# Optimization experiments

Measured on AMD Instinct MI355X. Metric: run time of the kernel, lower is better.

## Reference

```python
import jax, jax.numpy as jnp
import numpy as np

N, M, D = 8192, 2048, 32


def setup_inputs() -> dict:
    key = jax.random.key(0)
    k1, k2, k3 = jax.random.split(key, 3)
    samples = jax.random.normal(k1, (N, D), dtype=jnp.float32)
    means = jax.random.normal(k2, (M, D), dtype=jnp.float32)
    # stds are divisors; keep them strictly positive, in [0.5, 1.5)
    stds = jax.random.uniform(k3, (M, D), dtype=jnp.float32) + 0.5
    return {"samples": samples, "means": means, "stds": stds}


def reference(samples, means, stds):
    # [N, M, D] broadcast pairwise weighted squared distance (full-buffer KDE)
    diff = means[None, :, :] - samples[:, None, :]
    logp = -0.5 * jnp.sum(jnp.square(diff) / stds[None, :, :], axis=2)  # [N, M]
    dist = jnp.mean(jnp.exp(logp), axis=1)  # [N]
    # invert=True branch: flip the density around its midrange
    dist = -dist + jnp.max(dist) + jnp.min(dist)
    return dist
```

## Files before the change

### kernel.cpp

```cpp
#include <hip/hip_runtime.h>

#define NS 8192
#define MS 2048
#define DD 32
#define MSPLIT 16
#define MCH 128
#define NITS 8
#define RBLK 32

typedef __attribute__((ext_vector_type(8))) short bf16x8;
typedef __attribute__((ext_vector_type(4))) float f32x4;
typedef unsigned short u16;
typedef unsigned int u32;

#define PART_OFF 0
#define MM_OFF   (MSPLIT * NS * 4)
#define CNT_OFF  (MM_OFF + 8)

__device__ inline float fast_exp2(float x) {
#if __has_builtin(__builtin_amdgcn_exp2f)
    return __builtin_amdgcn_exp2f(x);
#else
    return exp2f(x);
#endif
}
__device__ inline float fast_rcp(float x) {
#if __has_builtin(__builtin_amdgcn_rcpf)
    return __builtin_amdgcn_rcpf(x);
#else
    return 1.0f / x;
#endif
}

__device__ inline u32 cvt_pk_bf16(float a, float b) {
    u32 r;
    asm("v_cvt_pk_bf16_f32 %0, %1, %2" : "=v"(r) : "v"(a), "v"(b));
    return r;
}

__device__ inline void split8(const float* v, bf16x8& hi, bf16x8& lo) {
    union { u32 u[4]; bf16x8 b; } H, L;
#pragma unroll
    for (int j = 0; j < 4; ++j) {
        u32 h = cvt_pk_bf16(v[2 * j], v[2 * j + 1]);
        float ha = __uint_as_float(h << 16);
        float hb = __uint_as_float(h & 0xFFFF0000u);
        L.u[j] = cvt_pk_bf16(v[2 * j] - ha, v[2 * j + 1] - hb);
        H.u[j] = h;
    }
    hi = H.b;
    lo = L.b;
}

__global__ __launch_bounds__(256, 4) void kde_fused(const float* __restrict__ samples,
                                                    const float* __restrict__ means,
                                                    const float* __restrict__ stds,
                                                    unsigned char* __restrict__ wsb) {
    __shared__ u16 WBH[NITS * 512], WBL[NITS * 512], WCH[NITS * 512], WCL[NITS * 512];
    __shared__ float A2s[MCH];

    const int t = threadIdx.x;
    const int m0 = blockIdx.y * MCH;
    const float L2E = 1.4426950408889634f;

    if (blockIdx.x == 0 && blockIdx.y == 0 && t == 0) {
        unsigned* mm = (unsigned*)(wsb + MM_OFF);
        mm[0] = 0x7f7fffffu;
        mm[1] = 0u;
        *(unsigned*)(wsb + CNT_OFF) = 0u;
    }

    {
        const int ml = t >> 1, half = t & 1, d0 = half * 16;
        const float* mp = means + (size_t)(m0 + ml) * DD + d0;
        const float* vp = stds  + (size_t)(m0 + ml) * DD + d0;
        float mu[16], sd[16];
#pragma unroll
        for (int j = 0; j < 4; ++j) {
            float4 a4 = *(const float4*)(mp + j * 4);
            float4 c4 = *(const float4*)(vp + j * 4);
            mu[j*4+0]=a4.x; mu[j*4+1]=a4.y; mu[j*4+2]=a4.z; mu[j*4+3]=a4.w;
            sd[j*4+0]=c4.x; sd[j*4+1]=c4.y; sd[j*4+2]=c4.z; sd[j*4+3]=c4.w;
        }
        float Bv[16], Cv[16], a = 0.f;
#pragma unroll
        for (int j = 0; j < 16; ++j) {
            float inv = fast_rcp(sd[j]);
            Bv[j] = L2E * mu[j] * inv;
            Cv[j] = -0.5f * L2E * inv;
            a += mu[j] * mu[j] * inv;
        }
        a += __shfl_xor(a, 1);
        if (half == 0) A2s[ml] = -0.5f * L2E * a - 11.0f;

        const int it = ml >> 4, r15 = ml & 15;
#pragma unroll
        for (int r2 = 0; r2 < 2; ++r2) {
            bf16x8 bh, bl, ch, cl;
            split8(Bv + r2 * 8, bh, bl);
            split8(Cv + r2 * 8, ch, cl);
            const int qd = half * 2 + r2;
            const int base = ((it * 4 + qd) * 16 + r15) * 8;
            *(bf16x8*)&WBH[base] = bh;
            *(bf16x8*)&WBL[base] = bl;
            *(bf16x8*)&WCH[base] = ch;
            *(bf16x8*)&WCL[base] = cl;
        }
    }

    const int lane = t & 63, wid = t >> 6;
    const int r15 = lane & 15, g = lane >> 4;
    const int n0 = blockIdx.x * 256 + wid * 64;

    bf16x8 xh[4], xl[4], qh[4], ql[4];
#pragma unroll
    for (int nt = 0; nt < 4; ++nt) {
        const float* sp = samples + (size_t)(n0 + nt * 16 + r15) * DD + g * 8;
        float4 a4 = *(const float4*)sp, b4 = *(const float4*)(sp + 4);
        float xv[8] = {a4.x, a4.y, a4.z, a4.w, b4.x, b4.y, b4.z, b4.w};
        float qv[8];
#pragma unroll
        for (int j = 0; j < 8; ++j) qv[j] = xv[j] * xv[j];
        split8(xv, xh[nt], xl[nt]);
        split8(qv, qh[nt], ql[nt]);
    }

    __syncthreads();

    float rs[4] = {0.f, 0.f, 0.f, 0.f};

#pragma unroll 2
    for (int it = 0; it < NITS; ++it) {
        const int base = ((it * 4 + g) * 16 + r15) * 8;
        bf16x8 bh = *(const bf16x8*)&WBH[base];
        bf16x8 ch = *(const bf16x8*)&WCH[base];
        bf16x8 bl = *(const bf16x8*)&WBL[base];
        bf16x8 cl = *(const bf16x8*)&WCL[base];
        const f32x4 a2v = *(const f32x4*)&A2s[it * 16 + g * 4];
#pragma unroll
        for (int nt = 0; nt < 4; ++nt) {
            f32x4 acc = a2v;
            acc = __builtin_amdgcn_mfma_f32_16x16x32_bf16(bh, xh[nt], acc, 0, 0, 0);
            acc = __builtin_amdgcn_mfma_f32_16x16x32_bf16(ch, qh[nt], acc, 0, 0, 0);
            acc = __builtin_amdgcn_mfma_f32_16x16x32_bf16(bh, xl[nt], acc, 0, 0, 0);
            acc = __builtin_amdgcn_mfma_f32_16x16x32_bf16(ch, ql[nt], acc, 0, 0, 0);
            acc = __builtin_amdgcn_mfma_f32_16x16x32_bf16(bl, xh[nt], acc, 0, 0, 0);
            acc = __builtin_amdgcn_mfma_f32_16x16x32_bf16(cl, qh[nt], acc, 0, 0, 0);
            rs[nt] += (fast_exp2(acc[0]) + fast_exp2(acc[1]))
                    + (fast_exp2(acc[2]) + fast_exp2(acc[3]));
        }
    }

#pragma unroll
    for (int nt = 0; nt < 4; ++nt) {
        rs[nt] += __shfl_xor(rs[nt], 16);
        rs[nt] += __shfl_xor(rs[nt], 32);
    }

    float* partial = (float*)(wsb + PART_OFF);
    if (g == 0) {
#pragma unroll
        for (int nt = 0; nt < 4; ++nt)
            partial[(size_t)blockIdx.y * NS + n0 + nt * 16 + r15] = rs[nt];
    }
}

__global__ __launch_bounds__(256) void reduce_flip(unsigned char* __restrict__ wsb,
                                                   float* __restrict__ out) {
    const float* partial = (const float*)(wsb + PART_OFF);
    unsigned* mm = (unsigned*)(wsb + MM_OFF);
    unsigned* cnt = (unsigned*)(wsb + CNT_OFF);

    const int tid = threadIdx.x;
    const int n = blockIdx.x * 256 + tid;
    float v = 0.f;
#pragma unroll
    for (int j = 0; j < MSPLIT; ++j) v += partial[(size_t)j * NS + n];

    float mn = v, mx = v;
#pragma unroll
    for (int o = 1; o < 64; o <<= 1) {
        mn = fminf(mn, __shfl_xor(mn, o));
        mx = fmaxf(mx, __shfl_xor(mx, o));
    }
    __shared__ float smn[4], smx[4];
    __shared__ float sres[2];
    const int wv = tid >> 6, ln = tid & 63;
    if (ln == 0) { smn[wv] = mn; smx[wv] = mx; }
    __syncthreads();
    if (tid == 0) {
#pragma unroll
        for (int j = 1; j < 4; ++j) {
            mn = fminf(mn, smn[j]);
            mx = fmaxf(mx, smx[j]);
        }
        atomicMin(mm + 0, __float_as_uint(mn));
        atomicMax(mm + 1, __float_as_uint(mx));
        __threadfence();
        atomicAdd(cnt, 1u);
        while (__hip_atomic_load(cnt, __ATOMIC_ACQUIRE, __HIP_MEMORY_SCOPE_AGENT)
               < RBLK) {}
        sres[0] = __uint_as_float(
            __hip_atomic_load(mm + 0, __ATOMIC_RELAXED, __HIP_MEMORY_SCOPE_AGENT));
        sres[1] = __uint_as_float(
            __hip_atomic_load(mm + 1, __ATOMIC_RELAXED, __HIP_MEMORY_SCOPE_AGENT));
    }
    __syncthreads();
    out[n] = sres[1] + sres[0] - v;
}

extern "C" void kernel_launch(void* const* d_in, const int* in_sizes, int n_in,
                              void* d_out, int out_size, void* d_ws, size_t ws_size,
                              hipStream_t stream) {
    const float* samples = (const float*)d_in[0];
    const float* means   = (const float*)d_in[1];
    const float* stds    = (const float*)d_in[2];
    unsigned char* ws = (unsigned char*)d_ws;
    float* out = (float*)d_out;

    kde_fused<<<dim3(NS / 256, MSPLIT), 256, 0, stream>>>(samples, means, stds, ws);
    reduce_flip<<<dim3(RBLK), 256, 0, stream>>>(ws, out);
}
```

Before: 17.14 us.

## Switch KDE distance MFMA from 16x16x32 to 32x32x16 bf16 tiles

Replaces the 16x16x32 bf16 MFMA tiling with 32x32x16 MFMAs. Each wave now covers 32 samples by 32 means per tile, with the K=32 feature dimension split into two halves. The LDS weight layout, sample register fragments, A2 bias broadcast and the final cross-lane reduction are all restructured to match the new operand layout. The intent is fewer MFMA issues, less operand traffic and fewer shuffles. In exchange it uses more accumulator registers, so launch bounds are lowered from 4 to 2 blocks per SM.

```diff
diff --git a/kernel.cpp b/kernel.cpp
--- a/kernel.cpp
+++ b/kernel.cpp
@@ -5,11 +5,12 @@
 #define DD 32
 #define MSPLIT 16
 #define MCH 128
-#define NITS 8
+#define NIT32 4
 #define RBLK 32
 
 typedef __attribute__((ext_vector_type(8))) short bf16x8;
 typedef __attribute__((ext_vector_type(4))) float f32x4;
+typedef __attribute__((ext_vector_type(16))) float f32x16;
 typedef unsigned short u16;
 typedef unsigned int u32;
 
@@ -52,11 +53,11 @@
     lo = L.b;
 }
 
-__global__ __launch_bounds__(256, 4) void kde_fused(const float* __restrict__ samples,
+__global__ __launch_bounds__(256, 2) void kde_fused(const float* __restrict__ samples,
                                                     const float* __restrict__ means,
                                                     const float* __restrict__ stds,
                                                     unsigned char* __restrict__ wsb) {
-    __shared__ u16 WBH[NITS * 512], WBL[NITS * 512], WCH[NITS * 512], WCL[NITS * 512];
+    __shared__ u16 WBH[4096], WBL[4096], WCH[4096], WCL[4096];
     __shared__ float A2s[MCH];
 
     const int t = threadIdx.x;
@@ -71,9 +72,9 @@
     }
 
     {
-        const int ml = t >> 1, half = t & 1, d0 = half * 16;
-        const float* mp = means + (size_t)(m0 + ml) * DD + d0;
-        const float* vp = stds  + (size_t)(m0 + ml) * DD + d0;
+        const int ml = t >> 1, c = t & 1;
+        const float* mp = means + (size_t)(m0 + ml) * DD + c * 16;
+        const float* vp = stds  + (size_t)(m0 + ml) * DD + c * 16;
         float mu[16], sd[16];
 #pragma unroll
         for (int j = 0; j < 4; ++j) {
@@ -91,16 +92,15 @@
             a += mu[j] * mu[j] * inv;
         }
         a += __shfl_xor(a, 1);
-        if (half == 0) A2s[ml] = -0.5f * L2E * a - 11.0f;
-
-        const int it = ml >> 4, r15 = ml & 15;
-#pragma unroll
-        for (int r2 = 0; r2 < 2; ++r2) {
+        if (c == 0) A2s[ml] = -0.5f * L2E * a - 11.0f;
+
+        const int it = ml >> 5, r31 = ml & 31;
+#pragma unroll
+        for (int h5 = 0; h5 < 2; ++h5) {
             bf16x8 bh, bl, ch, cl;
-            split8(Bv + r2 * 8, bh, bl);
-            split8(Cv + r2 * 8, ch, cl);
-            const int qd = half * 2 + r2;
-            const int base = ((it * 4 + qd) * 16 + r15) * 8;
+            split8(Bv + h5 * 8, bh, bl);
+            split8(Cv + h5 * 8, ch, cl);
+            const int base = (((it * 2 + c) * 2 + h5) * 32 + r31) * 8;
             *(bf16x8*)&WBH[base] = bh;
             *(bf16x8*)&WBL[base] = bl;
             *(bf16x8*)&WCH[base] = ch;
@@ -109,59 +109,85 @@
     }
 
     const int lane = t & 63, wid = t >> 6;
-    const int r15 = lane & 15, g = lane >> 4;
-    const int n0 = blockIdx.x * 256 + wid * 64;
-
-    bf16x8 xh[4], xl[4], qh[4], ql[4];
-#pragma unroll
-    for (int nt = 0; nt < 4; ++nt) {
-        const float* sp = samples + (size_t)(n0 + nt * 16 + r15) * DD + g * 8;
-        float4 a4 = *(const float4*)sp, b4 = *(const float4*)(sp + 4);
-        float xv[8] = {a4.x, a4.y, a4.z, a4.w, b4.x, b4.y, b4.z, b4.w};
-        float qv[8];
-#pragma unroll
-        for (int j = 0; j < 8; ++j) qv[j] = xv[j] * xv[j];
-        split8(xv, xh[nt], xl[nt]);
-        split8(qv, qh[nt], ql[nt]);
+    const int r31 = lane & 31, h5 = lane >> 5;
+    const int n0w = blockIdx.x * 256 + wid * 64;
+
+    bf16x8 xh[2][2], xl[2][2], qh[2][2], ql[2][2];
+#pragma unroll
+    for (int nt = 0; nt < 2; ++nt) {
+        const float* sp = samples + (size_t)(n0w + nt * 32 + r31) * DD;
+#pragma unroll
+        for (int c = 0; c < 2; ++c) {
+            const float* p = sp + c * 16 + h5 * 8;
+            float4 a4 = *(const float4*)p, b4 = *(const float4*)(p + 4);
+            float xv[8] = {a4.x, a4.y, a4.z, a4.w, b4.x, b4.y, b4.z, b4.w};
+            float qv[8];
+#pragma unroll
+            for (int j = 0; j < 8; ++j) qv[j] = xv[j] * xv[j];
+            split8(xv, xh[nt][c], xl[nt][c]);
+            split8(qv, qh[nt][c], ql[nt][c]);
+        }
     }
 
     __syncthreads();
 
-    float rs[4] = {0.f, 0.f, 0.f, 0.f};
+    float rs[2] = {0.f, 0.f};
 
 #pragma unroll 2
-    for (int it = 0; it < NITS; ++it) {
-        const int base = ((it * 4 + g) * 16 + r15) * 8;
-        bf16x8 bh = *(const bf16x8*)&WBH[base];
-        bf16x8 ch = *(const bf16x8*)&WCH[base];
-        bf16x8 bl = *(const bf16x8*)&WBL[base];
-        bf16x8 cl = *(const bf16x8*)&WCL[base];
-        const f32x4 a2v = *(const f32x4*)&A2s[it * 16 + g * 4];
-#pragma unroll
-        for (int nt = 0; nt < 4; ++nt) {
-            f32x4 acc = a2v;
-            acc = __builtin_amdgcn_mfma_f32_16x16x32_bf16(bh, xh[nt], acc, 0, 0, 0);
-            acc = __builtin_amdgcn_mfma_f32_16x16x32_bf16(ch, qh[nt], acc, 0, 0, 0);
-            acc = __builtin_amdgcn_mfma_f32_16x16x32_bf16(bh, xl[nt], acc, 0, 0, 0);
-            acc = __builtin_amdgcn_mfma_f32_16x16x32_bf16(ch, ql[nt], acc, 0, 0, 0);
-            acc = __builtin_amdgcn_mfma_f32_16x16x32_bf16(bl, xh[nt], acc, 0, 0, 0);
-            acc = __builtin_amdgcn_mfma_f32_16x16x32_bf16(cl, qh[nt], acc, 0, 0, 0);
-            rs[nt] += (fast_exp2(acc[0]) + fast_exp2(acc[1]))
-                    + (fast_exp2(acc[2]) + fast_exp2(acc[3]));
-        }
-    }
-
-#pragma unroll
-    for (int nt = 0; nt < 4; ++nt) {
-        rs[nt] += __shfl_xor(rs[nt], 16);
-        rs[nt] += __shfl_xor(rs[nt], 32);
-    }
+    for (int it = 0; it < NIT32; ++it) {
+        bf16x8 wbh[2], wch[2], wbl[2], wcl[2];
+#pragma unroll
+        for (int c = 0; c < 2; ++c) {
+            const int base = (((it * 2 + c) * 2 + h5) * 32 + r31) * 8;
+            wbh[c] = *(const bf16x8*)&WBH[base];
+            wch[c] = *(const bf16x8*)&WCH[base];
+            wbl[c] = *(const bf16x8*)&WBL[base];
+            wcl[c] = *(const bf16x8*)&WCL[base];
+        }
+        f32x4 a2v[4];
+#pragma unroll
+        for (int p = 0; p < 4; ++p)
+            a2v[p] = *(const f32x4*)&A2s[it * 32 + p * 8 + h5 * 4];
+
+#pragma unroll
+        for (int nt = 0; nt < 2; ++nt) {
+            f32x16 acc;
+#pragma unroll
+            for (int p = 0; p < 4; ++p)
+#pragma unroll
+                for (int q = 0; q < 4; ++q) acc[p * 4 + q] = a2v[p][q];
+
+            acc = __builtin_amdgcn_mfma_f32_32x32x16_bf16(wbh[0], xh[nt][0], acc, 0, 0, 0);
+            acc = __builtin_amdgcn_mfma_f32_32x32x16_bf16(wbh[1], xh[nt][1], acc, 0, 0, 0);
+            acc = __builtin_amdgcn_mfma_f32_32x32x16_bf16(wch[0], qh[nt][0], acc, 0, 0, 0);
+            acc = __builtin_amdgcn_mfma_f32_32x32x16_bf16(wch[1], qh[nt][1], acc, 0, 0, 0);
+            acc = __builtin_amdgcn_mfma_f32_32x32x16_bf16(wbh[0], xl[nt][0], acc, 0, 0, 0);
+            acc = __builtin_amdgcn_mfma_f32_32x32x16_bf16(wbh[1], xl[nt][1], acc, 0, 0, 0);
+            acc = __builtin_amdgcn_mfma_f32_32x32x16_bf16(wch[0], ql[nt][0], acc, 0, 0, 0);
+            acc = __builtin_amdgcn_mfma_f32_32x32x16_bf16(wch[1], ql[nt][1], acc, 0, 0, 0);
+            acc = __builtin_amdgcn_mfma_f32_32x32x16_bf16(wbl[0], xh[nt][0], acc, 0, 0, 0);
+            acc = __builtin_amdgcn_mfma_f32_32x32x16_bf16(wbl[1], xh[nt][1], acc, 0, 0, 0);
+            acc = __builtin_amdgcn_mfma_f32_32x32x16_bf16(wcl[0], qh[nt][0], acc, 0, 0, 0);
+            acc = __builtin_amdgcn_mfma_f32_32x32x16_bf16(wcl[1], qh[nt][1], acc, 0, 0, 0);
+
+            float e[16];
+#pragma unroll
+            for (int r = 0; r < 16; ++r) e[r] = fast_exp2(acc[r]);
+            rs[nt] += (((e[0] + e[1]) + (e[2] + e[3])) +
+                       ((e[4] + e[5]) + (e[6] + e[7]))) +
+                      (((e[8] + e[9]) + (e[10] + e[11])) +
+                       ((e[12] + e[13]) + (e[14] + e[15])));
+        }
+    }
+
+#pragma unroll
+    for (int nt = 0; nt < 2; ++nt) rs[nt] += __shfl_xor(rs[nt], 32);
 
     float* partial = (float*)(wsb + PART_OFF);
-    if (g == 0) {
-#pragma unroll
-        for (int nt = 0; nt < 4; ++nt)
-            partial[(size_t)blockIdx.y * NS + n0 + nt * 16 + r15] = rs[nt];
+    if (h5 == 0) {
+#pragma unroll
+        for (int nt = 0; nt < 2; ++nt)
+            partial[(size_t)blockIdx.y * NS + n0w + nt * 32 + r31] = rs[nt];
     }
 }
 
```

New measurement: 18.00 us. +5.0%, slower.
